# Kernel optimization log

Measured on AMD Instinct MI355X. Metric: run time of the kernel, lower is better.

The kernel has to match this reference:

```python
import jax, jax.numpy as jnp
import numpy as np

# Multi-level grid resolutions (module constants from init_kwargs)
RESO_3D = [16, 32, 64]
RESO_2D = [64, 128, 256]
EPS = 1e-9


def _corners(D):
    # binary corner offsets, shape (2**D, D)
    c = np.stack(np.meshgrid(*([np.arange(2)] * D), indexing='ij'), axis=-1).reshape(-1, D)
    return jnp.asarray(c, dtype=jnp.int32)


def _coords_weights(xyz, reso):
    # xyz in [0,1), shape (N, D). Returns flat voxel idx (N, 2**D) and trilinear weights (N, 2**D).
    D = xyz.shape[1]
    corners = _corners(D)                                   # (C, D)
    x = xyz * (reso - 1)
    x0 = jnp.floor(x)
    frac = x - x0                                           # (N, D)
    x0 = x0.astype(jnp.int32)
    cc = jnp.clip(x0[:, None, :] + corners[None], 0, reso - 1)   # (N, C, D)
    w = jnp.prod(jnp.where(corners[None] == 1, frac[:, None, :], 1.0 - frac[:, None, :]), axis=-1)  # (N, C)
    strides = (reso ** jnp.arange(D - 1, -1, -1)).astype(jnp.int32)  # row-major
    idx = jnp.sum(cc * strides, axis=-1)                    # (N, C)
    return idx, w


def _grid_create(xyz, feat, reso):
    # Scatter-splat: weighted-average point features into a dense level grid (reso**D, F).
    N, D = xyz.shape
    F = feat.shape[1]
    idx, w = _coords_weights(xyz, reso)                     # (N, C)
    flat_idx = idx.reshape(-1)
    wf = jnp.zeros((reso ** D, F), dtype=feat.dtype).at[flat_idx].add(
        (w[..., None] * feat[:, None, :]).reshape(-1, F))
    ws = jnp.zeros((reso ** D,), dtype=feat.dtype).at[flat_idx].add(w.reshape(-1))
    return wf / jnp.maximum(ws, EPS)[:, None]


def _grid_encode(xyz, grid, reso):
    # Gather + trilinear interpolation from a dense level grid. Returns (M, F).
    idx, w = _coords_weights(xyz, reso)                     # (M, C)
    vals = grid[idx]                                        # (M, C, F)
    return jnp.sum(w[..., None] * vals, axis=1)


def _spatial_ctx(xyz_c, xyz_i, feat):
    outs = []
    # 3D multi-level grid
    for R in RESO_3D:
        g = _grid_create(xyz_c, feat, R)
        outs.append(_grid_encode(xyz_i, g, R))
    # triplane 2D grids: xy, xz, yz
    for dims in ((0, 1), (0, 2), (1, 2)):
        xc = xyz_c[:, list(dims)]
        xi = xyz_i[:, list(dims)]
        for R in RESO_2D:
            g = _grid_create(xc, feat, R)
            outs.append(_grid_encode(xi, g, R))
    return jnp.concatenate(outs, axis=-1)  # (M, (L3 + 3*L2) * F)


def setup_inputs() -> dict:
    key = jax.random.key(0)
    k1, k2, k3 = jax.random.split(key, 3)
    N, M, F = 200000, 100000, 32
    xyz_for_creater = jax.random.uniform(k1, (N, 3), dtype=jnp.float32)
    xyz_for_interp = jax.random.uniform(k2, (M, 3), dtype=jnp.float32)
    feature = jax.random.normal(k3, (N, F), dtype=jnp.float32)
    return {"xyz_for_creater": xyz_for_creater,
            "xyz_for_interp": xyz_for_interp,
            "feature": feature}


def reference(xyz_for_creater, xyz_for_interp, feature):
    return _spatial_ctx(xyz_for_creater, xyz_for_interp, feature)
```

## Files before the change

kernel.cpp:

```cpp
#include <hip/hip_runtime.h>

#define NF 32
#define EPSF 1e-9f

#define KSORT 458752
#define KVIS 557056
#define KO16 0
#define KO32 4096
#define KO64 36864
#define KO64Q 299008
#define KO128Q 311296
#define KO256Q 360448

__device__ __forceinline__ int cell_coord(float xv, int R, float& fr) {
  float x = xv * (float)(R - 1);
  int i0 = (int)floorf(x);
  i0 = min(max(i0, 0), R - 2);
  fr = x - (float)i0;
  return i0;
}
__device__ __forceinline__ float bf2f(unsigned short u) {
  return __uint_as_float((unsigned)u << 16);
}
__device__ __forceinline__ unsigned short f2bf(float x) {
  unsigned b = __float_as_uint(x);
  return (unsigned short)((b + 0x7FFF + ((b >> 16) & 1)) >> 16);
}
__device__ __forceinline__ unsigned p1b2(unsigned x) {
  x &= 0x3FF;
  x = (x | (x << 16)) & 0x030000FF;
  x = (x | (x << 8)) & 0x0300F00F;
  x = (x | (x << 4)) & 0x030C30C3;
  x = (x | (x << 2)) & 0x09249249;
  return x;
}
__device__ __forceinline__ unsigned p1b1(unsigned x) {
  x &= 0xFFFF;
  x = (x | (x << 8)) & 0x00FF00FF;
  x = (x | (x << 4)) & 0x0F0F0F0F;
  x = (x | (x << 2)) & 0x33333333;
  x = (x | (x << 1)) & 0x55555555;
  return x;
}
__device__ __forceinline__ unsigned c1b2(unsigned x) {
  x &= 0x09249249u;
  x = (x | (x >> 2)) & 0x030C30C3u;
  x = (x | (x >> 4)) & 0x0300F00Fu;
  x = (x | (x >> 8)) & 0x030000FFu;
  x = (x | (x >> 16)) & 0x3FFu;
  return x;
}
__device__ __forceinline__ unsigned c1b1(unsigned x) {
  x &= 0x55555555u;
  x = (x | (x >> 1)) & 0x33333333u;
  x = (x | (x >> 2)) & 0x0F0F0F0Fu;
  x = (x | (x >> 4)) & 0x00FF00FFu;
  x = (x | (x >> 8)) & 0xFFFFu;
  return x;
}

__device__ __forceinline__ int xcd_swz(int bid, int n) {
  return (bid & 7) * (n >> 3) + (bid >> 3);
}

__device__ __forceinline__ void agg_hist(int key, int* cnt) {
  int lane = threadIdx.x & 63;
  unsigned long long amask = __ballot(1);
  int nact = __popcll(amask);
  int prev = __shfl_up(key, 1);
  bool leader = (lane == 0) || (prev != key);
  unsigned long long lmask = __ballot(leader);
  if (leader) {
    unsigned long long above = (lane < 63) ? (lmask >> (lane + 1)) : 0ULL;
    int next = above ? (lane + 1 + (__ffsll((unsigned long long)above) - 1)) : nact;
    atomicAdd(&cnt[key], next - lane);
  }
}
template <int NC>
__device__ __forceinline__ void agg_place_batch(const int (&key)[NC], int* cur,
                                                int (&pos)[NC]) {
  int lane = threadIdx.x & 63;
  unsigned long long amask = __ballot(1);
  int nact = __popcll(amask);
  int ret[NC];
  int lp[NC];
#pragma unroll
  for (int c = 0; c < NC; ++c) {
    int prev = __shfl_up(key[c], 1);
    bool leader = (lane == 0) || (prev != key[c]);
    unsigned long long lmask = __ballot(leader);
    unsigned long long below = lmask & ((2ULL << lane) - 1ULL);
    lp[c] = 63 - __clzll((long long)below);
    ret[c] = 0;
    if (leader) {
      unsigned long long above = (lane < 63) ? (lmask >> (lane + 1)) : 0ULL;
      int next = above ? (lane + 1 + (__ffsll((unsigned long long)above) - 1)) : nact;
      ret[c] = atomicAdd(&cur[key[c]], next - lane);
    }
  }
#pragma unroll
  for (int c = 0; c < NC; ++c) pos[c] = __shfl(ret[c], lp[c]) + (lane - lp[c]);
}

__global__ __launch_bounds__(256) void sort_hist_all(
    const float* __restrict__ xyz, int* __restrict__ cnt, int N) {
  int p = blockIdx.x * blockDim.x + threadIdx.x;
  if (p >= N) return;
  float fr;
  int c64[3], c256[3];
#pragma unroll
  for (int d = 0; d < 3; ++d) {
    c64[d] = cell_coord(xyz[p * 3 + d], 64, fr);
    c256[d] = cell_coord(xyz[p * 3 + d], 256, fr);
  }
  int k3 = (int)((p1b2((unsigned)c64[0]) << 2) | (p1b2((unsigned)c64[1]) << 1) |
                 p1b2((unsigned)c64[2]));
  atomicAdd(&cnt[k3], 1);
#pragma unroll
  for (int g = 0; g < 3; ++g) {
    int a = (g < 2) ? 0 : 1, b = (g == 0) ? 1 : 2;
    int key = 262144 + g * 65536 +
              (int)((p1b1((unsigned)c256[a]) << 1) | p1b1((unsigned)c256[b]));
    atomicAdd(&cnt[key], 1);
  }
}
__global__ __launch_bounds__(256) void sort_place_all(
    const float* __restrict__ xyz, int* __restrict__ cur, int* __restrict__ perm, int N) {
  int p = blockIdx.x * blockDim.x + threadIdx.x;
  if (p >= N) return;
  float fr;
  int c64[3], c256[3];
#pragma unroll
  for (int d = 0; d < 3; ++d) {
    c64[d] = cell_coord(xyz[p * 3 + d], 64, fr);
    c256[d] = cell_coord(xyz[p * 3 + d], 256, fr);
  }
  int k3 = (int)((p1b2((unsigned)c64[0]) << 2) | (p1b2((unsigned)c64[1]) << 1) |
                 p1b2((unsigned)c64[2]));
  perm[atomicAdd(&cur[k3], 1)] = p;
#pragma unroll
  for (int g = 0; g < 3; ++g) {
    int a = (g < 2) ? 0 : 1, b = (g == 0) ? 1 : 2;
    int key = 262144 + g * 65536 +
              (int)((p1b1((unsigned)c256[a]) << 1) | p1b1((unsigned)c256[b]));
    perm[atomicAdd(&cur[key], 1)] = p;
  }
}
__global__ __launch_bounds__(256) void permute_all(
    const float* __restrict__ xyz, const float* __restrict__ feat,
    const int* __restrict__ perm, float* __restrict__ xyz_s,
    unsigned short* __restrict__ feat_s, float* __restrict__ xy_g,
    unsigned short* __restrict__ feat_g, int N) {
  int t = blockIdx.x * blockDim.x + threadIdx.x;
  int s = t >> 5, f = t & 31;
  if (s >= 4 * N) return;
  int q = perm[s];
  float v = feat[(size_t)q * NF + f];
  if (s < N) {
    feat_s[(size_t)s * NF + f] = f2bf(v);
    if (f < 3) xyz_s[s * 3 + f] = xyz[q * 3 + f];
  } else {
    int sl = s - N;
    int g = sl / N;
    feat_g[(size_t)sl * NF + f] = f2bf(v);
    if (f < 2) {
      int a = (g < 2) ? 0 : 1, b = (g == 0) ? 1 : 2;
      xy_g[(size_t)sl * 2 + f] = xyz[q * 3 + (f == 0 ? a : b)];
    }
  }
}

__global__ __launch_bounds__(256) void scan_blocksum(
    const int* __restrict__ cnt, int* __restrict__ bsum, int K) {
  __shared__ int red[256];
  int base = blockIdx.x * 2048 + threadIdx.x * 8;
  int s = 0;
#pragma unroll
  for (int j = 0; j < 8; ++j) {
    int k = base + j;
    if (k < K) s += cnt[k];
  }
  red[threadIdx.x] = s;
  __syncthreads();
  for (int off = 128; off > 0; off >>= 1) {
    if (threadIdx.x < off) red[threadIdx.x] += red[threadIdx.x + off];
    __syncthreads();
  }
  if (threadIdx.x == 0) bsum[blockIdx.x] = red[0];
}
__global__ __launch_bounds__(256) void scan_write(
    const int* __restrict__ cnt, const int* __restrict__ bsum,
    int* __restrict__ cur, int K) {
  __shared__ int lds[256];
  __shared__ int boff;
  int b = blockIdx.x, t = threadIdx.x;
  if (t == 0) {
    int s = 0;
    for (int j = 0; j < b; ++j) s += bsum[j];
    boff = s;
  }
  int base = b * 2048 + t * 8;
  int v[8];
  int s = 0;
#pragma unroll
  for (int j = 0; j < 8; ++j) {
    int k = base + j;
    v[j] = (k < K) ? cnt[k] : 0;
    s += v[j];
  }
  lds[t] = s;
  __syncthreads();
  for (int off = 1; off < 256; off <<= 1) {
    int add = (t >= off) ? lds[t - off] : 0;
    __syncthreads();
    lds[t] += add;
    __syncthreads();
  }
  int run = boff + lds[t] - s;
#pragma unroll
  for (int j = 0; j < 8; ++j) {
    int k = base + j;
    if (k < K) {
      cur[k] = run;
      run += v[j];
    }
  }
}

__global__ __launch_bounds__(256) void hist_fused(
    const float* __restrict__ xyz_s, const float* __restrict__ xy_g,
    int* __restrict__ cnt, int N) {
  int y = blockIdx.y;
  int p = blockIdx.x * blockDim.x + threadIdx.x;
  if (p >= N) return;
  if (y < 2) {
    int R = 16 << y;
    int ko = (y == 0) ? KO16 : KO32;
    unsigned a0[3], a1[3];
    float fr[3];
#pragma unroll
    for (int d = 0; d < 3; ++d) {
      int i0 = cell_coord(xyz_s[p * 3 + d], R, fr[d]);
      a0[d] = p1b2((unsigned)i0);
      a1[d] = p1b2((unsigned)(i0 + 1));
    }
#pragma unroll
    for (int cb = 0; cb < 8; ++cb) {
      unsigned key = 0;
#pragma unroll
      for (int d = 0; d < 3; ++d) {
        int o = (cb >> d) & 1;
        key |= (o ? a1[d] : a0[d]) << (2 - d);
      }
      agg_hist(ko + (int)key, cnt);
    }
  } else {
    int idx = y - 2;
    int g = idx >> 1, r = idx & 1;
    int sl = g * N + p;
    int R = 64 << r;
    int kb = (r == 0) ? KO64Q : KO128Q;
    int base = kb + g * R * R;
    float frx, fry;
    int ix = cell_coord(xy_g[(size_t)sl * 2 + 0], R, frx);
    int iy = cell_coord(xy_g[(size_t)sl * 2 + 1], R, fry);
    unsigned ax0 = p1b1((unsigned)ix), ax1 = p1b1((unsigned)(ix + 1));
    unsigned ay0 = p1b1((unsigned)iy), ay1 = p1b1((unsigned)(iy + 1));
#pragma unroll
    for (int cb = 0; cb < 4; ++cb) {
      int o0 = (cb >> 1) & 1, o1 = cb & 1;
      agg_hist(base + (int)(((o0 ? ax1 : ax0) << 1) | (o1 ? ay1 : ay0)), cnt);
    }
  }
}

__global__ __launch_bounds__(256) void place_fused(
    const float* __restrict__ xyz_s, const float* __restrict__ xy_g,
    const int* __restrict__ cnt_all, const int* __restrict__ cur_all,
    int* __restrict__ cur_v, const int* __restrict__ coff3,
    const int* __restrict__ coff2, int2* __restrict__ visits, int N) {
  int y = blockIdx.y;
  int p = blockIdx.x * blockDim.x + threadIdx.x;
  if (p >= N) return;
  if (y < 2) {
    int R = 16 << y;
    int ko = (y == 0) ? KO16 : KO32;
    unsigned a0[3], a1[3];
    float fr[3];
#pragma unroll
    for (int d = 0; d < 3; ++d) {
      int i0 = cell_coord(xyz_s[p * 3 + d], R, fr[d]);
      a0[d] = p1b2((unsigned)i0);
      a1[d] = p1b2((unsigned)(i0 + 1));
    }
    int keys[8];
    float ws[8];
#pragma unroll
    for (int cb = 0; cb < 8; ++cb) {
      float w = 1.f;
      unsigned key = 0;
#pragma unroll
      for (int d = 0; d < 3; ++d) {
        int o = (cb >> d) & 1;
        w *= o ? fr[d] : (1.f - fr[d]);
        key |= (o ? a1[d] : a0[d]) << (2 - d);
      }
      keys[cb] = ko + (int)key;
      ws[cb] = w;
    }
    int pos[8];
    agg_place_batch<8>(keys, cur_v, pos);
#pragma unroll
    for (int cb = 0; cb < 8; ++cb)
      visits[pos[cb]] = make_int2(p, __float_as_int(ws[cb]));
  } else if (y < 8) {
    int idx = y - 2;
    int g = idx >> 1, r = idx & 1;
    int sl = g * N + p;
    int R = 64 << r;
    int kb = (r == 0) ? KO64Q : KO128Q;
    int base = kb + g * R * R;
    float frx, fry;
    int ix = cell_coord(xy_g[(size_t)sl * 2 + 0], R, frx);
    int iy = cell_coord(xy_g[(size_t)sl * 2 + 1], R, fry);
    unsigned ax0 = p1b1((unsigned)ix), ax1 = p1b1((unsigned)(ix + 1));
    unsigned ay0 = p1b1((unsigned)iy), ay1 = p1b1((unsigned)(iy + 1));
    int keys[4];
    float ws[4];
#pragma unroll
    for (int cb = 0; cb < 4; ++cb) {
      int o0 = (cb >> 1) & 1, o1 = cb & 1;
      ws[cb] = (o0 ? frx : 1.f - frx) * (o1 ? fry : 1.f - fry);
      keys[cb] = base + (int)(((o0 ? ax1 : ax0) << 1) | (o1 ? ay1 : ay0));
    }
    int pos[4];
    agg_place_batch<4>(keys, cur_v, pos);
#pragma unroll
    for (int cb = 0; cb < 4; ++cb)
      visits[pos[cb]] = make_int2(sl, __float_as_int(ws[cb]));
  } else if (y == 8) {
    unsigned a0[3], a1[3];
    float fr[3];
#pragma unroll
    for (int d = 0; d < 3; ++d) {
      int i0 = cell_coord(xyz_s[p * 3 + d], 64, fr[d]);
      a0[d] = p1b2((unsigned)i0);
      a1[d] = p1b2((unsigned)(i0 + 1));
    }
    int hk = (int)((a0[0] << 2) | (a0[1] << 1) | a0[2]);
    int rank = p - (cur_all[hk] - cnt_all[hk]);
#pragma unroll
    for (int cb = 0; cb < 8; ++cb) {
      float w = 1.f;
      unsigned key = 0;
#pragma unroll
      for (int d = 0; d < 3; ++d) {
        int o = (cb >> d) & 1;
        w *= o ? fr[d] : (1.f - fr[d]);
        key |= (o ? a1[d] : a0[d]) << (2 - d);
      }
      int pos = coff3[(size_t)key * 8 + cb] + rank;
      visits[pos] = make_int2(p, __float_as_int(w));
    }
  } else {
    int g = y - 9;
    int sl = g * N + p;
    float frx, fry;
    int ix = cell_coord(xy_g[(size_t)sl * 2 + 0], 256, frx);
    int iy = cell_coord(xy_g[(size_t)sl * 2 + 1], 256, fry);
    unsigned ax0 = p1b1((unsigned)ix), ax1 = p1b1((unsigned)(ix + 1));
    unsigned ay0 = p1b1((unsigned)iy), ay1 = p1b1((unsigned)(iy + 1));
    int m = (int)((ax0 << 1) | ay0);
    int sk = 262144 + g * 65536 + m;
    int rank = sl - (cur_all[sk] - cnt_all[sk] - N);
#pragma unroll
    for (int cb = 0; cb < 4; ++cb) {
      int o0 = (cb >> 1) & 1, o1 = cb & 1;
      float w = (o0 ? frx : 1.f - frx) * (o1 ? fry : 1.f - fry);
      int key = (int)(((o0 ? ax1 : ax0) << 1) | (o1 ? ay1 : ay0));
      int pos = coff2[(size_t)(g * 65536 + key) * 4 + cb] + rank;
      visits[pos] = make_int2(sl, __float_as_int(w));
    }
  }
}

__global__ __launch_bounds__(256) void stencilA_all(const int* __restrict__ cnt_all,
                                                    int* __restrict__ cnt_v) {
  int t = blockIdx.x * 256 + threadIdx.x;
  if (t < 262144) {
    int c = t;
    int cx = (int)c1b2((unsigned)c >> 2), cy = (int)c1b2((unsigned)c >> 1),
        cz = (int)c1b2((unsigned)c);
    int s = 0;
#pragma unroll
    for (int cls = 0; cls < 8; ++cls) {
      int hx = cx - (cls & 1), hy = cy - ((cls >> 1) & 1), hz = cz - ((cls >> 2) & 1);
      if (hx < 0 || hy < 0 || hz < 0) continue;
      s += cnt_all[(int)((p1b2((unsigned)hx) << 2) | (p1b2((unsigned)hy) << 1) |
                         p1b2((unsigned)hz))];
    }
    cnt_v[KO64 + c] = s;
  } else {
    int t2 = t - 262144;
    int g = t2 >> 16, m = t2 & 65535;
    int cx = (int)c1b1((unsigned)m >> 1), cy = (int)c1b1((unsigned)m);
    const int* h = cnt_all + 262144 + g * 65536;
    int s = 0;
#pragma unroll
    for (int cls = 0; cls < 4; ++cls) {
      int hx = cx - ((cls >> 1) & 1), hy = cy - (cls & 1);
      if (hx < 0 || hy < 0) continue;
      s += h[(int)((p1b1((unsigned)hx) << 1) | p1b1((unsigned)hy))];
    }
    cnt_v[KO256Q + t2] = s;
  }
}
__global__ __launch_bounds__(256) void stencilB_all(const int* __restrict__ cnt_all,
                                                    const int* __restrict__ cur_v,
                                                    int* __restrict__ coff3,
                                                    int* __restrict__ coff2) {
  int t = blockIdx.x * 256 + threadIdx.x;
  if (t < 262144) {
    int c = t;
    int cx = (int)c1b2((unsigned)c >> 2), cy = (int)c1b2((unsigned)c >> 1),
        cz = (int)c1b2((unsigned)c);
    int run = cur_v[KO64 + c];
#pragma unroll
    for (int cls = 0; cls < 8; ++cls) {
      coff3[(size_t)c * 8 + cls] = run;
      int hx = cx - (cls & 1), hy = cy - ((cls >> 1) & 1), hz = cz - ((cls >> 2) & 1);
      if (hx < 0 || hy < 0 || hz < 0) continue;
      run += cnt_all[(int)((p1b2((unsigned)hx) << 2) | (p1b2((unsigned)hy) << 1) |
                           p1b2((unsigned)hz))];
    }
  } else {
    int t2 = t - 262144;
    int g = t2 >> 16, m = t2 & 65535;
    int cx = (int)c1b1((unsigned)m >> 1), cy = (int)c1b1((unsigned)m);
    const int* h = cnt_all + 262144 + g * 65536;
    int run = cur_v[KO256Q + t2];
#pragma unroll
    for (int cls = 0; cls < 4; ++cls) {
      coff2[(size_t)t2 * 4 + cls] = run;
      int hx = cx - ((cls >> 1) & 1), hy = cy - (cls & 1);
      if (hx < 0 || hy < 0) continue;
      run += h[(int)((p1b1((unsigned)hx) << 1) | p1b1((unsigned)hy))];
    }
  }
}

__global__ __launch_bounds__(256) void create_block_fused(
    const unsigned short* __restrict__ feat_s, const unsigned short* __restrict__ feat_g,
    const int* __restrict__ cnt, const int* __restrict__ cur_end,
    const int2* __restrict__ visits, unsigned short* __restrict__ grid) {
  __shared__ int2 vlds[1024];
  __shared__ float2 lacc[256];
  __shared__ float lw[16];
  int bid = blockIdx.x;
  int ko, base, nseg;
  const unsigned short* feat;
  if (bid < 4096) {
    ko = KO16; base = 0; nseg = 4096; feat = feat_s;
  } else if (bid < 36864) {
    ko = KO32; base = 4096; nseg = 32768; feat = feat_s;
  } else if (bid < 49152) {
    ko = KO64Q; base = 36864; nseg = 12288; feat = feat_g;
  } else {
    ko = KO128Q; base = 49152; nseg = 49152; feat = feat_g;
  }
  int cell = ko + xcd_swz(bid - base, nseg);
  int e = cur_end[cell];
  int n = cnt[cell];
  int beg = e - n;
  for (int i = threadIdx.x; i < n && i < 1024; i += 256) vlds[i] = visits[beg + i];
  __syncthreads();
  bool inl = (n <= 1024);
  int slot = threadIdx.x >> 4;
  int fp = threadIdx.x & 15;
  float2 acc = {0.f, 0.f};
  float wsum = 0.f;
  int i = slot;
  for (; i + 16 < n; i += 32) {
    int2 v0 = inl ? vlds[i] : visits[beg + i];
    int2 v1 = inl ? vlds[i + 16] : visits[beg + i + 16];
    unsigned u0 = *(const unsigned*)(feat + (size_t)v0.x * NF + 2 * fp);
    unsigned u1 = *(const unsigned*)(feat + (size_t)v1.x * NF + 2 * fp);
    float w0 = __int_as_float(v0.y), w1 = __int_as_float(v1.y);
    acc.x = fmaf(w0, bf2f((unsigned short)u0), acc.x);
    acc.y = fmaf(w0, bf2f((unsigned short)(u0 >> 16)), acc.y);
    acc.x = fmaf(w1, bf2f((unsigned short)u1), acc.x);
    acc.y = fmaf(w1, bf2f((unsigned short)(u1 >> 16)), acc.y);
    wsum += w0 + w1;
  }
  if (i < n) {
    int2 v = inl ? vlds[i] : visits[beg + i];
    unsigned u = *(const unsigned*)(feat + (size_t)v.x * NF + 2 * fp);
    float w = __int_as_float(v.y);
    acc.x = fmaf(w, bf2f((unsigned short)u), acc.x);
    acc.y = fmaf(w, bf2f((unsigned short)(u >> 16)), acc.y);
    wsum += w;
  }
  lacc[threadIdx.x] = acc;
  if (fp == 0) lw[slot] = wsum;
  __syncthreads();
  if (threadIdx.x < 16) {
    float2 a = {0.f, 0.f};
    float w = 0.f;
#pragma unroll
    for (int s = 0; s < 16; ++s) {
      float2 t = lacc[s * 16 + threadIdx.x];
      a.x += t.x;
      a.y += t.y;
      w += lw[s];
    }
    float inv = 1.f / fmaxf(w, EPSF);
    unsigned short lo = f2bf(a.x * inv), hi = f2bf(a.y * inv);
    *(unsigned*)(grid + (size_t)cell * NF + 2 * threadIdx.x) =
        (unsigned)lo | ((unsigned)hi << 16);
  }
}

__global__ __launch_bounds__(256) void create_wave_fused(
    const unsigned short* __restrict__ feat_s, const unsigned short* __restrict__ feat_g,
    const int* __restrict__ cnt, const int* __restrict__ cur_start,
    const int2* __restrict__ visits, unsigned short* __restrict__ grid) {
  __shared__ int2 vlds[1024];
  int bid = blockIdx.x;
  int ko, base, nblk, K;
  const unsigned short* feat;
  if (bid < 65536) {
    ko = KO64; base = 0; nblk = 65536; K = 262144; feat = feat_s;
  } else {
    ko = KO256Q; base = 65536; nblk = 49152; K = 196608; feat = feat_g;
  }
  int wave = threadIdx.x >> 6, lane = threadIdx.x & 63;
  int slot = lane >> 4;
  int fp = lane & 15;
  int c0 = ko + xcd_swz(bid - base, nblk) * 4;
  int lastc = min(c0 + 3, ko + K - 1);
  int vbase = cur_start[c0];
  int vlen = cur_start[lastc] + cnt[lastc] - vbase;
  for (int i = threadIdx.x; i < vlen && i < 1024; i += 256) vlds[i] = visits[vbase + i];
  __syncthreads();
  int cell = c0 + wave;
  if (cell > lastc) return;
  int beg = cur_start[cell];
  int n = cnt[cell];
  bool inl = (beg + n - vbase) <= 1024;
  int b0 = beg - vbase;
  float2 acc = {0.f, 0.f};
  float wsum = 0.f;
  for (int i = slot; i < n; i += 4) {
    int2 v = inl ? vlds[b0 + i] : visits[beg + i];
    unsigned u = *(const unsigned*)(feat + (size_t)v.x * NF + 2 * fp);
    float w = __int_as_float(v.y);
    acc.x = fmaf(w, bf2f((unsigned short)u), acc.x);
    acc.y = fmaf(w, bf2f((unsigned short)(u >> 16)), acc.y);
    wsum += w;
  }
  acc.x += __shfl_xor(acc.x, 16);
  acc.y += __shfl_xor(acc.y, 16);
  wsum += __shfl_xor(wsum, 16);
  acc.x += __shfl_xor(acc.x, 32);
  acc.y += __shfl_xor(acc.y, 32);
  wsum += __shfl_xor(wsum, 32);
  if (slot == 0) {
    float inv = 1.f / fmaxf(wsum, EPSF);
    unsigned short lo = f2bf(acc.x * inv), hi = f2bf(acc.y * inv);
    *(unsigned*)(grid + (size_t)cell * NF + 2 * fp) =
        (unsigned)lo | ((unsigned)hi << 16);
  }
}

__global__ __launch_bounds__(256) void encode_all(
    const float* __restrict__ xyz, const unsigned short* __restrict__ grid,
    float* __restrict__ out, int M) {
  int t = blockIdx.x * blockDim.x + threadIdx.x;
  int m = t >> 5, f = t & 31;
  if (m >= M) return;
  float X[3];
#pragma unroll
  for (int d = 0; d < 3; ++d) X[d] = xyz[m * 3 + d];
  {
    const int RS[3] = {16, 32, 64};
    const int KO[3] = {KO16, KO32, KO64};
#pragma unroll
    for (int r = 0; r < 3; ++r) {
      unsigned a0[3], a1[3];
      float fr[3];
#pragma unroll
      for (int d = 0; d < 3; ++d) {
        int i0 = cell_coord(X[d], RS[r], fr[d]);
        a0[d] = p1b2((unsigned)i0);
        a1[d] = p1b2((unsigned)(i0 + 1));
      }
      float acc = 0.f;
#pragma unroll
      for (int cb = 0; cb < 8; ++cb) {
        float w = 1.f;
        unsigned key = 0;
#pragma unroll
        for (int d = 0; d < 3; ++d) {
          int o = (cb >> d) & 1;
          w *= o ? fr[d] : (1.f - fr[d]);
          key |= (o ? a1[d] : a0[d]) << (2 - d);
        }
        acc = fmaf(w, bf2f(grid[(size_t)(KO[r] + (int)key) * NF + f]), acc);
      }
      out[(size_t)m * 384 + r * 32 + f] = acc;
    }
  }
  {
    const int RS[3] = {64, 128, 256};
    const int KB[3] = {KO64Q, KO128Q, KO256Q};
    const int RSQ[3] = {4096, 16384, 65536};
#pragma unroll
    for (int r = 0; r < 3; ++r) {
      unsigned b0[3], b1[3];
      float fr[3];
#pragma unroll
      for (int d = 0; d < 3; ++d) {
        int i0 = cell_coord(X[d], RS[r], fr[d]);
        b0[d] = p1b1((unsigned)i0);
        b1[d] = p1b1((unsigned)(i0 + 1));
      }
#pragma unroll
      for (int g = 0; g < 3; ++g) {
        int a = (g < 2) ? 0 : 1, b = (g == 0) ? 1 : 2;
        int base = KB[r] + g * RSQ[r];
        float acc = 0.f;
#pragma unroll
        for (int cb = 0; cb < 4; ++cb) {
          int o0 = (cb >> 1) & 1, o1 = cb & 1;
          float w = (o0 ? fr[a] : 1.f - fr[a]) * (o1 ? fr[b] : 1.f - fr[b]);
          int k = base + (int)(((o0 ? b1[a] : b0[a]) << 1) | (o1 ? b1[b] : b0[b]));
          acc = fmaf(w, bf2f(grid[(size_t)k * NF + f]), acc);
        }
        out[(size_t)m * 384 + (3 + g * 3 + r) * 32 + f] = acc;
      }
    }
  }
}

extern "C" void kernel_launch(void* const* d_in, const int* in_sizes, int n_in,
                              void* d_out, int out_size, void* d_ws, size_t ws_size,
                              hipStream_t stream) {
  const float* xyz_c = (const float*)d_in[0];
  const float* xyz_i = (const float*)d_in[1];
  const float* feat = (const float*)d_in[2];
  float* out = (float*)d_out;
  int N = in_sizes[0] / 3;
  int M = in_sizes[1] / 3;

  char* wsb = (char*)d_ws;
  size_t off = 0;
  auto al = [&](size_t bytes) {
    size_t o = off;
    off = (off + bytes + 255) & ~(size_t)255;
    return wsb + o;
  };
  const int KALL = KSORT + KVIS;
  int* cnt_all = (int*)al((size_t)KALL * 4);
  int* cur_all = (int*)al((size_t)KALL * 4);
  int* bsum = (int*)al(4096);
  int* perm = (int*)al((size_t)4 * N * 4);
  float* xyz_s = (float*)al((size_t)N * 3 * 4);
  unsigned short* feat_s = (unsigned short*)al((size_t)N * NF * 2);
  float* xy_g = (float*)al((size_t)3 * N * 2 * 4);
  unsigned short* feat_g = (unsigned short*)al((size_t)3 * N * NF * 2);
  int2* visits = (int2*)al((size_t)60 * N * 8);
  unsigned short* grid = (unsigned short*)al((size_t)KVIS * NF * 2);
  int* coff3 = (int*)al((size_t)262144 * 8 * 4);
  int* coff2 = (int*)al((size_t)196608 * 4 * 4);

  int* cnt_v = cnt_all + KSORT;
  int* cur_v = cur_all + KSORT;

  int pb = (N + 255) / 256;
  int nbs = (KSORT + 2047) / 2048;
  int nbv = (KVIS + 2047) / 2048;

  hipMemsetAsync(cnt_all, 0, (size_t)KALL * 4, stream);

  sort_hist_all<<<pb, 256, 0, stream>>>(xyz_c, cnt_all, N);
  scan_blocksum<<<nbs, 256, 0, stream>>>(cnt_all, bsum, KSORT);
  scan_write<<<nbs, 256, 0, stream>>>(cnt_all, bsum, cur_all, KSORT);
  sort_place_all<<<pb, 256, 0, stream>>>(xyz_c, cur_all, perm, N);
  permute_all<<<(4 * N * 32 + 255) / 256, 256, 0, stream>>>(xyz_c, feat, perm, xyz_s,
                                                            feat_s, xy_g, feat_g, N);

  hist_fused<<<dim3(pb, 8), 256, 0, stream>>>(xyz_s, xy_g, cnt_v, N);
  stencilA_all<<<(KSORT) / 256, 256, 0, stream>>>(cnt_all, cnt_v);
  scan_blocksum<<<nbv, 256, 0, stream>>>(cnt_v, bsum, KVIS);
  scan_write<<<nbv, 256, 0, stream>>>(cnt_v, bsum, cur_v, KVIS);
  stencilB_all<<<(KSORT) / 256, 256, 0, stream>>>(cnt_all, cur_v, coff3, coff2);

  place_fused<<<dim3(pb, 12), 256, 0, stream>>>(xyz_s, xy_g, cnt_all, cur_all, cur_v,
                                                coff3, coff2, visits, N);

  create_block_fused<<<98304, 256, 0, stream>>>(feat_s, feat_g, cnt_v, cur_v, visits,
                                                grid);
  create_wave_fused<<<114688, 256, 0, stream>>>(feat_s, feat_g, cnt_v, cur_v, visits,
                                                grid);

  encode_all<<<(M * 32 + 255) / 256, 256, 0, stream>>>(xyz_i, grid, out, M);
}
```

Measured before the change: 786.1 us.

## Compute fine-level splats directly from sorted points, dropping visit lists

For the 64^3 and 256^2 levels, the visit-list construction is removed: the stencil kernels, the coff tables and the fine-level placement passes no longer exist. Each output cell now walks its neighbouring sorted-point buckets through the existing sort histogram and recomputes the trilinear weights from the sorted coordinates. This cuts several kernel launches, the scan size and visit memory traffic. In exchange, each cell does a per-iteration bucket lookup and re-reads coordinates, so the same points are fetched by up to 8 (3D) or 4 (2D) neighbouring cells.

```diff
diff --git a/kernel.cpp b/kernel.cpp
--- a/kernel.cpp
+++ b/kernel.cpp
@@ -4,13 +4,18 @@
 #define EPSF 1e-9f
 
 #define KSORT 458752
-#define KVIS 557056
+#define VO16 0
+#define VO32 4096
+#define VO64Q 36864
+#define VO128Q 49152
+#define KVIS2 98304
 #define KO16 0
 #define KO32 4096
 #define KO64 36864
 #define KO64Q 299008
 #define KO128Q 311296
 #define KO256Q 360448
+#define KVIS 557056
 
 __device__ __forceinline__ int cell_coord(float xv, int R, float& fr) {
   float x = xv * (float)(R - 1);
@@ -235,7 +240,7 @@
   if (p >= N) return;
   if (y < 2) {
     int R = 16 << y;
-    int ko = (y == 0) ? KO16 : KO32;
+    int ko = (y == 0) ? VO16 : VO32;
     unsigned a0[3], a1[3];
     float fr[3];
 #pragma unroll
@@ -259,7 +264,7 @@
     int g = idx >> 1, r = idx & 1;
     int sl = g * N + p;
     int R = 64 << r;
-    int kb = (r == 0) ? KO64Q : KO128Q;
+    int kb = (r == 0) ? VO64Q : VO128Q;
     int base = kb + g * R * R;
     float frx, fry;
     int ix = cell_coord(xy_g[(size_t)sl * 2 + 0], R, frx);
@@ -276,15 +281,13 @@
 
 __global__ __launch_bounds__(256) void place_fused(
     const float* __restrict__ xyz_s, const float* __restrict__ xy_g,
-    const int* __restrict__ cnt_all, const int* __restrict__ cur_all,
-    int* __restrict__ cur_v, const int* __restrict__ coff3,
-    const int* __restrict__ coff2, int2* __restrict__ visits, int N) {
+    int* __restrict__ cur_v, int2* __restrict__ visits, int N) {
   int y = blockIdx.y;
   int p = blockIdx.x * blockDim.x + threadIdx.x;
   if (p >= N) return;
   if (y < 2) {
     int R = 16 << y;
-    int ko = (y == 0) ? KO16 : KO32;
+    int ko = (y == 0) ? VO16 : VO32;
     unsigned a0[3], a1[3];
     float fr[3];
 #pragma unroll
@@ -313,12 +316,12 @@
 #pragma unroll
     for (int cb = 0; cb < 8; ++cb)
       visits[pos[cb]] = make_int2(p, __float_as_int(ws[cb]));
-  } else if (y < 8) {
+  } else {
     int idx = y - 2;
     int g = idx >> 1, r = idx & 1;
     int sl = g * N + p;
     int R = 64 << r;
-    int kb = (r == 0) ? KO64Q : KO128Q;
+    int kb = (r == 0) ? VO64Q : VO128Q;
     int base = kb + g * R * R;
     float frx, fry;
     int ix = cell_coord(xy_g[(size_t)sl * 2 + 0], R, frx);
@@ -338,114 +341,6 @@
 #pragma unroll
     for (int cb = 0; cb < 4; ++cb)
       visits[pos[cb]] = make_int2(sl, __float_as_int(ws[cb]));
-  } else if (y == 8) {
-    unsigned a0[3], a1[3];
-    float fr[3];
-#pragma unroll
-    for (int d = 0; d < 3; ++d) {
-      int i0 = cell_coord(xyz_s[p * 3 + d], 64, fr[d]);
-      a0[d] = p1b2((unsigned)i0);
-      a1[d] = p1b2((unsigned)(i0 + 1));
-    }
-    int hk = (int)((a0[0] << 2) | (a0[1] << 1) | a0[2]);
-    int rank = p - (cur_all[hk] - cnt_all[hk]);
-#pragma unroll
-    for (int cb = 0; cb < 8; ++cb) {
-      float w = 1.f;
-      unsigned key = 0;
-#pragma unroll
-      for (int d = 0; d < 3; ++d) {
-        int o = (cb >> d) & 1;
-        w *= o ? fr[d] : (1.f - fr[d]);
-        key |= (o ? a1[d] : a0[d]) << (2 - d);
-      }
-      int pos = coff3[(size_t)key * 8 + cb] + rank;
-      visits[pos] = make_int2(p, __float_as_int(w));
-    }
-  } else {
-    int g = y - 9;
-    int sl = g * N + p;
-    float frx, fry;
-    int ix = cell_coord(xy_g[(size_t)sl * 2 + 0], 256, frx);
-    int iy = cell_coord(xy_g[(size_t)sl * 2 + 1], 256, fry);
-    unsigned ax0 = p1b1((unsigned)ix), ax1 = p1b1((unsigned)(ix + 1));
-    unsigned ay0 = p1b1((unsigned)iy), ay1 = p1b1((unsigned)(iy + 1));
-    int m = (int)((ax0 << 1) | ay0);
-    int sk = 262144 + g * 65536 + m;
-    int rank = sl - (cur_all[sk] - cnt_all[sk] - N);
-#pragma unroll
-    for (int cb = 0; cb < 4; ++cb) {
-      int o0 = (cb >> 1) & 1, o1 = cb & 1;
-      float w = (o0 ? frx : 1.f - frx) * (o1 ? fry : 1.f - fry);
-      int key = (int)(((o0 ? ax1 : ax0) << 1) | (o1 ? ay1 : ay0));
-      int pos = coff2[(size_t)(g * 65536 + key) * 4 + cb] + rank;
-      visits[pos] = make_int2(sl, __float_as_int(w));
-    }
-  }
-}
-
-__global__ __launch_bounds__(256) void stencilA_all(const int* __restrict__ cnt_all,
-                                                    int* __restrict__ cnt_v) {
-  int t = blockIdx.x * 256 + threadIdx.x;
-  if (t < 262144) {
-    int c = t;
-    int cx = (int)c1b2((unsigned)c >> 2), cy = (int)c1b2((unsigned)c >> 1),
-        cz = (int)c1b2((unsigned)c);
-    int s = 0;
-#pragma unroll
-    for (int cls = 0; cls < 8; ++cls) {
-      int hx = cx - (cls & 1), hy = cy - ((cls >> 1) & 1), hz = cz - ((cls >> 2) & 1);
-      if (hx < 0 || hy < 0 || hz < 0) continue;
-      s += cnt_all[(int)((p1b2((unsigned)hx) << 2) | (p1b2((unsigned)hy) << 1) |
-                         p1b2((unsigned)hz))];
-    }
-    cnt_v[KO64 + c] = s;
-  } else {
-    int t2 = t - 262144;
-    int g = t2 >> 16, m = t2 & 65535;
-    int cx = (int)c1b1((unsigned)m >> 1), cy = (int)c1b1((unsigned)m);
-    const int* h = cnt_all + 262144 + g * 65536;
-    int s = 0;
-#pragma unroll
-    for (int cls = 0; cls < 4; ++cls) {
-      int hx = cx - ((cls >> 1) & 1), hy = cy - (cls & 1);
-      if (hx < 0 || hy < 0) continue;
-      s += h[(int)((p1b1((unsigned)hx) << 1) | p1b1((unsigned)hy))];
-    }
-    cnt_v[KO256Q + t2] = s;
-  }
-}
-__global__ __launch_bounds__(256) void stencilB_all(const int* __restrict__ cnt_all,
-                                                    const int* __restrict__ cur_v,
-                                                    int* __restrict__ coff3,
-                                                    int* __restrict__ coff2) {
-  int t = blockIdx.x * 256 + threadIdx.x;
-  if (t < 262144) {
-    int c = t;
-    int cx = (int)c1b2((unsigned)c >> 2), cy = (int)c1b2((unsigned)c >> 1),
-        cz = (int)c1b2((unsigned)c);
-    int run = cur_v[KO64 + c];
-#pragma unroll
-    for (int cls = 0; cls < 8; ++cls) {
-      coff3[(size_t)c * 8 + cls] = run;
-      int hx = cx - (cls & 1), hy = cy - ((cls >> 1) & 1), hz = cz - ((cls >> 2) & 1);
-      if (hx < 0 || hy < 0 || hz < 0) continue;
-      run += cnt_all[(int)((p1b2((unsigned)hx) << 2) | (p1b2((unsigned)hy) << 1) |
-                           p1b2((unsigned)hz))];
-    }
-  } else {
-    int t2 = t - 262144;
-    int g = t2 >> 16, m = t2 & 65535;
-    int cx = (int)c1b1((unsigned)m >> 1), cy = (int)c1b1((unsigned)m);
-    const int* h = cnt_all + 262144 + g * 65536;
-    int run = cur_v[KO256Q + t2];
-#pragma unroll
-    for (int cls = 0; cls < 4; ++cls) {
-      coff2[(size_t)t2 * 4 + cls] = run;
-      int hx = cx - ((cls >> 1) & 1), hy = cy - (cls & 1);
-      if (hx < 0 || hy < 0) continue;
-      run += h[(int)((p1b1((unsigned)hx) << 1) | p1b1((unsigned)hy))];
-    }
   }
 }
 
@@ -457,20 +352,21 @@
   __shared__ float2 lacc[256];
   __shared__ float lw[16];
   int bid = blockIdx.x;
-  int ko, base, nseg;
+  int vo, go, base, nseg;
   const unsigned short* feat;
   if (bid < 4096) {
-    ko = KO16; base = 0; nseg = 4096; feat = feat_s;
+    vo = VO16; go = KO16; base = 0; nseg = 4096; feat = feat_s;
   } else if (bid < 36864) {
-    ko = KO32; base = 4096; nseg = 32768; feat = feat_s;
+    vo = VO32; go = KO32; base = 4096; nseg = 32768; feat = feat_s;
   } else if (bid < 49152) {
-    ko = KO64Q; base = 36864; nseg = 12288; feat = feat_g;
+    vo = VO64Q; go = KO64Q; base = 36864; nseg = 12288; feat = feat_g;
   } else {
-    ko = KO128Q; base = 49152; nseg = 49152; feat = feat_g;
-  }
-  int cell = ko + xcd_swz(bid - base, nseg);
-  int e = cur_end[cell];
-  int n = cnt[cell];
+    vo = VO128Q; go = KO128Q; base = 49152; nseg = 49152; feat = feat_g;
+  }
+  int idx = xcd_swz(bid - base, nseg);
+  int vcell = vo + idx;
+  int e = cur_end[vcell];
+  int n = cnt[vcell];
   int beg = e - n;
   for (int i = threadIdx.x; i < n && i < 1024; i += 256) vlds[i] = visits[beg + i];
   __syncthreads();
@@ -515,48 +411,102 @@
     }
     float inv = 1.f / fmaxf(w, EPSF);
     unsigned short lo = f2bf(a.x * inv), hi = f2bf(a.y * inv);
-    *(unsigned*)(grid + (size_t)cell * NF + 2 * threadIdx.x) =
+    *(unsigned*)(grid + (size_t)(go + idx) * NF + 2 * threadIdx.x) =
         (unsigned)lo | ((unsigned)hi << 16);
   }
 }
 
-__global__ __launch_bounds__(256) void create_wave_fused(
-    const unsigned short* __restrict__ feat_s, const unsigned short* __restrict__ feat_g,
-    const int* __restrict__ cnt, const int* __restrict__ cur_start,
-    const int2* __restrict__ visits, unsigned short* __restrict__ grid) {
-  __shared__ int2 vlds[1024];
+__global__ __launch_bounds__(256) void create_direct_fused(
+    const float* __restrict__ xyz_s, const unsigned short* __restrict__ feat_s,
+    const float* __restrict__ xy_g, const unsigned short* __restrict__ feat_g,
+    const int* __restrict__ cnt_all, const int* __restrict__ cur_all,
+    unsigned short* __restrict__ grid, int N) {
   int bid = blockIdx.x;
-  int ko, base, nblk, K;
-  const unsigned short* feat;
-  if (bid < 65536) {
-    ko = KO64; base = 0; nblk = 65536; K = 262144; feat = feat_s;
-  } else {
-    ko = KO256Q; base = 65536; nblk = 49152; K = 196608; feat = feat_g;
-  }
   int wave = threadIdx.x >> 6, lane = threadIdx.x & 63;
   int slot = lane >> 4;
   int fp = lane & 15;
-  int c0 = ko + xcd_swz(bid - base, nblk) * 4;
-  int lastc = min(c0 + 3, ko + K - 1);
-  int vbase = cur_start[c0];
-  int vlen = cur_start[lastc] + cnt[lastc] - vbase;
-  for (int i = threadIdx.x; i < vlen && i < 1024; i += 256) vlds[i] = visits[vbase + i];
-  __syncthreads();
-  int cell = c0 + wave;
-  if (cell > lastc) return;
-  int beg = cur_start[cell];
-  int n = cnt[cell];
-  bool inl = (beg + n - vbase) <= 1024;
-  int b0 = beg - vbase;
   float2 acc = {0.f, 0.f};
   float wsum = 0.f;
-  for (int i = slot; i < n; i += 4) {
-    int2 v = inl ? vlds[b0 + i] : visits[beg + i];
-    unsigned u = *(const unsigned*)(feat + (size_t)v.x * NF + 2 * fp);
-    float w = __int_as_float(v.y);
-    acc.x = fmaf(w, bf2f((unsigned short)u), acc.x);
-    acc.y = fmaf(w, bf2f((unsigned short)(u >> 16)), acc.y);
-    wsum += w;
+  int gcell;
+  if (bid < 65536) {
+    int cell = xcd_swz(bid, 65536) * 4 + wave;
+    gcell = KO64 + cell;
+    int cx = (int)c1b2((unsigned)cell >> 2);
+    int cy = (int)c1b2((unsigned)cell >> 1);
+    int cz = (int)c1b2((unsigned)cell);
+    int beg[8], pre[8];
+    int tot = 0;
+#pragma unroll
+    for (int cb = 0; cb < 8; ++cb) {
+      pre[cb] = tot;
+      int hx = cx - (cb & 1), hy = cy - ((cb >> 1) & 1), hz = cz - ((cb >> 2) & 1);
+      int n = 0, b = 0;
+      if (hx >= 0 && hy >= 0 && hz >= 0) {
+        int hk = (int)((p1b2((unsigned)hx) << 2) | (p1b2((unsigned)hy) << 1) |
+                       p1b2((unsigned)hz));
+        n = cnt_all[hk];
+        b = cur_all[hk] - n;
+      }
+      beg[cb] = b;
+      tot += n;
+    }
+    for (int i = slot; i < tot; i += 4) {
+      int cls = 0, b = beg[0], p0 = pre[0];
+#pragma unroll
+      for (int c2 = 1; c2 < 8; ++c2) {
+        if (i >= pre[c2]) { cls = c2; b = beg[c2]; p0 = pre[c2]; }
+      }
+      int q = b + (i - p0);
+      int hx = cx - (cls & 1), hy = cy - ((cls >> 1) & 1), hz = cz - ((cls >> 2) & 1);
+      float frx = xyz_s[q * 3 + 0] * 63.0f - (float)hx;
+      float fry = xyz_s[q * 3 + 1] * 63.0f - (float)hy;
+      float frz = xyz_s[q * 3 + 2] * 63.0f - (float)hz;
+      float w = ((cls & 1) ? frx : 1.f - frx) * (((cls >> 1) & 1) ? fry : 1.f - fry) *
+                (((cls >> 2) & 1) ? frz : 1.f - frz);
+      unsigned u = *(const unsigned*)(feat_s + (size_t)q * NF + 2 * fp);
+      acc.x = fmaf(w, bf2f((unsigned short)u), acc.x);
+      acc.y = fmaf(w, bf2f((unsigned short)(u >> 16)), acc.y);
+      wsum += w;
+    }
+  } else {
+    int cl = xcd_swz(bid - 65536, 49152) * 4 + wave;
+    gcell = KO256Q + cl;
+    int g = cl >> 16, m = cl & 65535;
+    int cx = (int)c1b1((unsigned)m >> 1);
+    int cy = (int)c1b1((unsigned)m);
+    const int* cntg = cnt_all + 262144 + g * 65536;
+    const int* curg = cur_all + 262144 + g * 65536;
+    int beg[4], pre[4];
+    int tot = 0;
+#pragma unroll
+    for (int cb = 0; cb < 4; ++cb) {
+      pre[cb] = tot;
+      int hx = cx - ((cb >> 1) & 1), hy = cy - (cb & 1);
+      int n = 0, b = 0;
+      if (hx >= 0 && hy >= 0) {
+        int hk = (int)((p1b1((unsigned)hx) << 1) | p1b1((unsigned)hy));
+        n = cntg[hk];
+        b = curg[hk] - n - N;
+      }
+      beg[cb] = b;
+      tot += n;
+    }
+    for (int i = slot; i < tot; i += 4) {
+      int cls = 0, b = beg[0], p0 = pre[0];
+#pragma unroll
+      for (int c2 = 1; c2 < 4; ++c2) {
+        if (i >= pre[c2]) { cls = c2; b = beg[c2]; p0 = pre[c2]; }
+      }
+      int q = b + (i - p0);
+      int hx = cx - ((cls >> 1) & 1), hy = cy - (cls & 1);
+      float frx = xy_g[(size_t)q * 2 + 0] * 255.0f - (float)hx;
+      float fry = xy_g[(size_t)q * 2 + 1] * 255.0f - (float)hy;
+      float w = (((cls >> 1) & 1) ? frx : 1.f - frx) * ((cls & 1) ? fry : 1.f - fry);
+      unsigned u = *(const unsigned*)(feat_g + (size_t)q * NF + 2 * fp);
+      acc.x = fmaf(w, bf2f((unsigned short)u), acc.x);
+      acc.y = fmaf(w, bf2f((unsigned short)(u >> 16)), acc.y);
+      wsum += w;
+    }
   }
   acc.x += __shfl_xor(acc.x, 16);
   acc.y += __shfl_xor(acc.y, 16);
@@ -567,7 +517,7 @@
   if (slot == 0) {
     float inv = 1.f / fmaxf(wsum, EPSF);
     unsigned short lo = f2bf(acc.x * inv), hi = f2bf(acc.y * inv);
-    *(unsigned*)(grid + (size_t)cell * NF + 2 * fp) =
+    *(unsigned*)(grid + (size_t)gcell * NF + 2 * fp) =
         (unsigned)lo | ((unsigned)hi << 16);
   }
 }
@@ -659,7 +609,7 @@
     off = (off + bytes + 255) & ~(size_t)255;
     return wsb + o;
   };
-  const int KALL = KSORT + KVIS;
+  const int KALL = KSORT + KVIS2;
   int* cnt_all = (int*)al((size_t)KALL * 4);
   int* cur_all = (int*)al((size_t)KALL * 4);
   int* bsum = (int*)al(4096);
@@ -668,17 +618,15 @@
   unsigned short* feat_s = (unsigned short*)al((size_t)N * NF * 2);
   float* xy_g = (float*)al((size_t)3 * N * 2 * 4);
   unsigned short* feat_g = (unsigned short*)al((size_t)3 * N * NF * 2);
-  int2* visits = (int2*)al((size_t)60 * N * 8);
+  int2* visits = (int2*)al((size_t)40 * N * 8);
   unsigned short* grid = (unsigned short*)al((size_t)KVIS * NF * 2);
-  int* coff3 = (int*)al((size_t)262144 * 8 * 4);
-  int* coff2 = (int*)al((size_t)196608 * 4 * 4);
 
   int* cnt_v = cnt_all + KSORT;
   int* cur_v = cur_all + KSORT;
 
   int pb = (N + 255) / 256;
   int nbs = (KSORT + 2047) / 2048;
-  int nbv = (KVIS + 2047) / 2048;
+  int nbv = (KVIS2 + 2047) / 2048;
 
   hipMemsetAsync(cnt_all, 0, (size_t)KALL * 4, stream);
 
@@ -690,18 +638,14 @@
                                                             feat_s, xy_g, feat_g, N);
 
   hist_fused<<<dim3(pb, 8), 256, 0, stream>>>(xyz_s, xy_g, cnt_v, N);
-  stencilA_all<<<(KSORT) / 256, 256, 0, stream>>>(cnt_all, cnt_v);
-  scan_blocksum<<<nbv, 256, 0, stream>>>(cnt_v, bsum, KVIS);
-  scan_write<<<nbv, 256, 0, stream>>>(cnt_v, bsum, cur_v, KVIS);
-  stencilB_all<<<(KSORT) / 256, 256, 0, stream>>>(cnt_all, cur_v, coff3, coff2);
-
-  place_fused<<<dim3(pb, 12), 256, 0, stream>>>(xyz_s, xy_g, cnt_all, cur_all, cur_v,
-                                                coff3, coff2, visits, N);
+  scan_blocksum<<<nbv, 256, 0, stream>>>(cnt_v, bsum, KVIS2);
+  scan_write<<<nbv, 256, 0, stream>>>(cnt_v, bsum, cur_v, KVIS2);
+  place_fused<<<dim3(pb, 8), 256, 0, stream>>>(xyz_s, xy_g, cur_v, visits, N);
 
   create_block_fused<<<98304, 256, 0, stream>>>(feat_s, feat_g, cnt_v, cur_v, visits,
                                                 grid);
-  create_wave_fused<<<114688, 256, 0, stream>>>(feat_s, feat_g, cnt_v, cur_v, visits,
-                                                grid);
+  create_direct_fused<<<114688, 256, 0, stream>>>(xyz_s, feat_s, xy_g, feat_g, cnt_all,
+                                                  cur_all, grid, N);
 
   encode_all<<<(M * 32 + 255) / 256, 256, 0, stream>>>(xyz_i, grid, out, M);
 }
```

Measured after the change: 831.3 us. 5.7% more time.
